# Kernel optimization log

Hardware: AMD Instinct MI355X
Metric: run time of the kernel (lower is better)

Reference implementation:

```python
import jax, jax.numpy as jnp
import numpy as np

EMB = 256
HEADS = 4
HD = EMB // HEADS
BS, SZ = 4, 64


def _layernorm(x, g, b, eps=1e-5):
    mu = jnp.mean(x, axis=-1, keepdims=True)
    var = jnp.mean((x - mu) ** 2, axis=-1, keepdims=True)
    return (x - mu) * jax.lax.rsqrt(var + eps) * g + b


def setup_inputs() -> dict:
    key = jax.random.key(0)
    ks = jax.random.split(key, 12)
    s = lambda k, shape, sc: jax.random.normal(k, shape, jnp.float32) * sc
    return {
        "x": s(ks[0], (BS, EMB, SZ, SZ), 1.0),
        "ln1_g": jnp.ones((EMB,), jnp.float32),
        "ln1_b": jnp.zeros((EMB,), jnp.float32),
        "wq": s(ks[1], (HD, HD), HD ** -0.5), "bq": jnp.zeros((HD,), jnp.float32),
        "wk": s(ks[2], (HD, HD), HD ** -0.5), "bk": jnp.zeros((HD,), jnp.float32),
        "wv": s(ks[3], (HD, HD), HD ** -0.5), "bv": jnp.zeros((HD,), jnp.float32),
        "wo": s(ks[4], (EMB, EMB), EMB ** -0.5), "bo": jnp.zeros((EMB,), jnp.float32),
        "ln2_g": jnp.ones((EMB,), jnp.float32),
        "ln2_b": jnp.zeros((EMB,), jnp.float32),
        "w1": s(ks[5], (EMB, EMB), EMB ** -0.5), "b1": jnp.zeros((EMB,), jnp.float32),
        "w2": s(ks[6], (EMB, EMB), EMB ** -0.5), "b2": jnp.zeros((EMB,), jnp.float32),
    }


def reference(x, ln1_g, ln1_b, wq, bq, wk, bk, wv, bv, wo, bo, ln2_g, ln2_b, w1, b1, w2, b2):
    bs, c, sz, _ = x.shape
    seq = sz * sz
    xt = x.reshape(bs, c, seq).swapaxes(1, 2)  # [b, s, c]
    xn = _layernorm(xt, ln1_g, ln1_b)
    # split heads: [b, h, s, d]
    h = xn.reshape(bs, seq, HEADS, HD).transpose(0, 2, 1, 3)
    q = h @ wq + bq
    k = h @ wk + bk
    v = h @ wv + bv
    scores = jnp.einsum("bhqd,bhkd->bhqk", q, k) / (HD ** 0.5)
    attn = jax.nn.softmax(scores, axis=-1)
    o = jnp.einsum("bhqk,bhkd->bhqd", attn, v)
    o = o.transpose(0, 2, 1, 3).reshape(bs, seq, c)
    o = o @ wo + bo
    av = o + xt  # residual 1
    ff = _layernorm(av, ln2_g, ln2_b) @ w1 + b1
    ff = jax.nn.gelu(ff, approximate=False) @ w2 + b2
    out = ff + av  # residual 2
    return out.swapaxes(1, 2).reshape(bs, c, sz, sz)
```

## Files before the change

kernel.cpp:

```cpp
#include <hip/hip_runtime.h>
#include <hip/hip_bf16.h>
#include <cstdint>

typedef __attribute__((ext_vector_type(8))) short short8;
typedef __attribute__((ext_vector_type(4))) short short4_;
typedef __attribute__((ext_vector_type(4))) float float4_;

#define MFMA16(a,b,c)  __builtin_amdgcn_mfma_f32_16x16x32_bf16(a,b,c,0,0,0)
#define MFMA16K16(a,b,c) __builtin_amdgcn_mfma_f32_16x16x16bf16_1k(a,b,c,0,0,0)
#define EXP2(x) __builtin_amdgcn_exp2f(x)

__device__ __forceinline__ short f2bs(float f) {
    union { float f; uint32_t u; } c;
    c.f = f;
    c.u += 0x7FFF + ((c.u >> 16) & 1);
    return (short)(c.u >> 16);
}
__device__ __forceinline__ float s2f(short s) {
    union { uint32_t u; float f; } c;
    c.u = ((uint32_t)(uint16_t)s) << 16;
    return c.f;
}

static const int EMB = 256;
static const int SEQ = 4096;
static const int TOK = 16384;

static const size_t SZO = 4194304;
static const size_t LSTRIDE = 65536;

#define QSCALE 0.18033688011112042f

__global__ __launch_bounds__(256) void repack_kernel(
    const float* wq, const float* wk, const float* wv,
    const float* wo, const float* w1, const float* w2,
    short* wqT, short* wkT, short* wvT, short* woT, short* w1T, short* w2T)
{
    int idx = blockIdx.x * 256 + threadIdx.x;
    if (idx < 3 * 4096) {
        int m = idx / 4096, r = idx % 4096;
        int n = r / 64, k = r % 64;
        const float* src = (m == 0) ? wq : (m == 1) ? wk : wv;
        short* dst = (m == 0) ? wqT : (m == 1) ? wkT : wvT;
        float v = src[k * 64 + n];
        if (m == 0) v *= QSCALE;
        dst[n * 64 + k] = f2bs(v);
    } else {
        int idx2 = idx - 3 * 4096;
        if (idx2 < 3 * 65536) {
            int m = idx2 / 65536, r = idx2 % 65536;
            int n = r / 256, k = r % 256;
            const float* src = (m == 0) ? wo : (m == 1) ? w1 : w2;
            short* dst = (m == 0) ? woT : (m == 1) ? w1T : w2T;
            dst[n * 256 + k] = f2bs(src[k * 256 + n]);
        }
    }
}

__global__ __launch_bounds__(256) void ln1_kernel(
    const float* x, const float* g, const float* bta,
    short* xn, short* xt)
{
    __shared__ float redS[4][32], redQ[4][32];
    int tid = threadIdx.x;
    int l = tid & 31;
    int p = tid >> 5;
    int t = blockIdx.x * 32 + l;
    int b = t >> 12, sp = t & 4095;
    const float* xb = x + (size_t)b * EMB * SEQ + (size_t)(p * 32) * SEQ + sp;

    float v[32];
    float sum = 0.f, ss = 0.f;
#pragma unroll
    for (int j = 0; j < 32; j++) {
        v[j] = xb[(size_t)j * SEQ];
        sum += v[j]; ss += v[j] * v[j];
    }
    sum += __shfl_xor(sum, 32);
    ss  += __shfl_xor(ss, 32);
    int w = tid >> 6;
    if ((tid & 32) == 0) { redS[w][l] = sum; redQ[w][l] = ss; }
    __syncthreads();
    float S = (redS[0][l] + redS[1][l]) + (redS[2][l] + redS[3][l]);
    float Q = (redQ[0][l] + redQ[1][l]) + (redQ[2][l] + redQ[3][l]);
    float mu = S * (1.f / 256.f);
    float var = Q * (1.f / 256.f) - mu * mu;
    float rs = rsqrtf(var + 1e-5f);

    short* xnr = xn + (size_t)t * 256 + p * 32;
    short* xtr = xt + (size_t)t * 256 + p * 32;
#pragma unroll
    for (int c = 0; c < 32; c += 8) {
        short8 ra, na;
#pragma unroll
        for (int j = 0; j < 8; j++) {
            float vv = v[c + j];
            ra[j] = f2bs(vv);
            na[j] = f2bs((vv - mu) * rs * g[p * 32 + c + j] + bta[p * 32 + c + j]);
        }
        *(short8*)(xtr + c) = ra;
        *(short8*)(xnr + c) = na;
    }
}

__global__ __launch_bounds__(256) void qkv_kernel(
    const short* xn, const short* wqT, const short* wkT, const short* wvT,
    const float* bq, const float* bk, const float* bv,
    short* qo, short* ko, short* vto)
{
    int tid = threadIdx.x;
    int w = tid >> 6, lane = tid & 63, quad = lane >> 4, l15 = lane & 15;
    int m0 = blockIdx.x * 64 + w * 16;
    int row = m0 + l15;
    int bb = row >> 12;
    int p = blockIdx.y;

    short8 a0[4], a1[4];
#pragma unroll
    for (int h = 0; h < 4; h++) {
        a0[h] = *(const short8*)(xn + (size_t)row * 256 + h * 64 + quad * 8);
        a1[h] = *(const short8*)(xn + (size_t)row * 256 + h * 64 + 32 + quad * 8);
    }

    const short* WT = (p == 0) ? wqT : (p == 1) ? wkT : wvT;
    const float* bias = (p == 0) ? bq : (p == 1) ? bk : bv;

    if (p < 2) {
        float bscale = (p == 0) ? QSCALE : 1.f;
        short* dst = (p == 0) ? qo : ko;
        int s0 = (m0 & 4095) + quad * 4;
#pragma unroll
        for (int nb = 0; nb < 4; nb++) {
            int col = nb * 16 + l15;
            short8 b0 = *(const short8*)(WT + col * 64 + quad * 8);
            short8 b1 = *(const short8*)(WT + col * 64 + 32 + quad * 8);
            float bvv = bias[col] * bscale;
#pragma unroll
            for (int h = 0; h < 4; h++) {
                float4_ acc = {bvv, bvv, bvv, bvv};
                acc = MFMA16(a0[h], b0, acc);
                acc = MFMA16(a1[h], b1, acc);
                size_t headbase = (size_t)(bb * 4 + h) * SEQ;
#pragma unroll
                for (int r = 0; r < 4; r++)
                    dst[(headbase + s0 + r) * 64 + col] = f2bs(acc[r]);
            }
        }
    } else {
        int sp0 = m0 & 4095;
#pragma unroll
        for (int nb = 0; nb < 4; nb++) {
            int colw = nb * 16 + l15;
            short8 b0 = *(const short8*)(WT + colw * 64 + quad * 8);
            short8 b1 = *(const short8*)(WT + colw * 64 + 32 + quad * 8);
            float4_ binit;
#pragma unroll
            for (int r = 0; r < 4; r++) binit[r] = bias[nb * 16 + quad * 4 + r];
#pragma unroll
            for (int h = 0; h < 4; h++) {
                float4_ acc = binit;
                acc = MFMA16(b0, a0[h], acc);
                acc = MFMA16(b1, a1[h], acc);
                size_t dbase = ((size_t)(bb * 4 + h) * 64 + nb * 16 + quad * 4) * SEQ;
#pragma unroll
                for (int r = 0; r < 4; r++)
                    vto[dbase + (size_t)r * SEQ + sp0 + l15] = f2bs(acc[r]);
            }
        }
    }
}

__global__ __attribute__((amdgpu_flat_work_group_size(256, 256),
                          amdgpu_waves_per_eu(4, 4)))
void flash_kernel(
    const short* q, const short* k, const short* vt,
    short* O0, short* Orest, float* lbase)
{
    __shared__ short K_lds[64 * 64];
    __shared__ short V_lds[64 * 64];

    int tid = threadIdx.x;
    int w = tid >> 6, lane = tid & 63, quad = lane >> 4, l15 = lane & 15;
    int qt = blockIdx.x, bh = blockIdx.y, grp = blockIdx.z;
    int span = 64 / gridDim.z;

    const short* qb = q + (size_t)bh * SEQ * 64;
    const short* kb = k + (size_t)bh * SEQ * 64 + (size_t)grp * span * 64 * 64;
    const short* vb = vt + (size_t)bh * 64 * SEQ + grp * span * 64;

    int qrow0 = qt * 128 + w * 32 + l15;
    int qrow1 = qrow0 + 16;
    short8 qA0 = *(const short8*)(qb + (size_t)qrow0 * 64 + quad * 8);
    short8 qA1 = *(const short8*)(qb + (size_t)qrow0 * 64 + 32 + quad * 8);
    short8 qB0 = *(const short8*)(qb + (size_t)qrow1 * 64 + quad * 8);
    short8 qB1 = *(const short8*)(qb + (size_t)qrow1 * 64 + 32 + quad * 8);

    float4_ oacc0[4], oacc1[4];
#pragma unroll
    for (int md = 0; md < 4; md++) {
        oacc0[md] = {0.f, 0.f, 0.f, 0.f};
        oacc1[md] = {0.f, 0.f, 0.f, 0.f};
    }
    float li0 = 0.f, li1 = 0.f;

    int srow = tid >> 2;
    int c0 = tid & 3;
    int sw = (srow & 7) ^ ((srow & 1) << 2);
    int rw = (l15 & 7) ^ ((l15 & 1) << 2);

    int dcA = (c0 ^ sw) << 3;
    int dcB = ((c0 + 4) ^ sw) << 3;

    short8 kr0 = *(const short8*)(kb + (size_t)srow * 64 + c0 * 8);
    short8 kr1 = *(const short8*)(kb + (size_t)srow * 64 + (c0 + 4) * 8);
    short8 vr0 = *(const short8*)(vb + (size_t)srow * SEQ + c0 * 8);
    short8 vr1 = *(const short8*)(vb + (size_t)srow * SEQ + (c0 + 4) * 8);

    for (int kt = 0; kt < span; kt++) {
        __syncthreads();
        *(short8*)&K_lds[srow * 64 + dcA] = kr0;
        *(short8*)&K_lds[srow * 64 + dcB] = kr1;
        *(short8*)&V_lds[srow * 64 + dcA] = vr0;
        *(short8*)&V_lds[srow * 64 + dcB] = vr1;
        if (kt + 1 < span) {
            kr0 = *(const short8*)(kb + (size_t)((kt + 1) * 64 + srow) * 64 + c0 * 8);
            kr1 = *(const short8*)(kb + (size_t)((kt + 1) * 64 + srow) * 64 + (c0 + 4) * 8);
            vr0 = *(const short8*)(vb + (size_t)srow * SEQ + (kt + 1) * 64 + c0 * 8);
            vr1 = *(const short8*)(vb + (size_t)srow * SEQ + (kt + 1) * 64 + (c0 + 4) * 8);
        }
        asm volatile("s_waitcnt lgkmcnt(0)" ::: "memory");
        __builtin_amdgcn_s_barrier();
        asm volatile("" ::: "memory");

        short4_ pf0[4], pf1[4];
#pragma unroll
        for (int nb = 0; nb < 4; nb++) {
            short8 k0 = *(const short8*)&K_lds[(nb * 16 + l15) * 64 + ((quad ^ rw) << 3)];
            short8 k1 = *(const short8*)&K_lds[(nb * 16 + l15) * 64 + (((quad + 4) ^ rw) << 3)];
            float4_ a = {0.f, 0.f, 0.f, 0.f};
            a = MFMA16(k0, qA0, a);
            a = MFMA16(k1, qA1, a);
            float4_ b = {0.f, 0.f, 0.f, 0.f};
            b = MFMA16(k0, qB0, b);
            b = MFMA16(k1, qB1, b);

            float p00 = EXP2(a[0]), p01 = EXP2(a[1]);
            float p02 = EXP2(a[2]), p03 = EXP2(a[3]);
            li0 += (p00 + p01) + (p02 + p03);
            float p10 = EXP2(b[0]), p11 = EXP2(b[1]);
            float p12 = EXP2(b[2]), p13 = EXP2(b[3]);
            li1 += (p10 + p11) + (p12 + p13);
            union { short4_ s; uint32_t u[2]; } pa, pb;
            asm("v_cvt_pk_bf16_f32 %0, %1, %2" : "=v"(pa.u[0]) : "v"(p00), "v"(p01));
            asm("v_cvt_pk_bf16_f32 %0, %1, %2" : "=v"(pa.u[1]) : "v"(p02), "v"(p03));
            asm("v_cvt_pk_bf16_f32 %0, %1, %2" : "=v"(pb.u[0]) : "v"(p10), "v"(p11));
            asm("v_cvt_pk_bf16_f32 %0, %1, %2" : "=v"(pb.u[1]) : "v"(p12), "v"(p13));
            pf0[nb] = pa.s;
            pf1[nb] = pb.s;
        }

        __builtin_amdgcn_s_setprio(1);
#pragma unroll
        for (int md = 0; md < 4; md++)
#pragma unroll
            for (int nb = 0; nb < 4; nb++) {
                int c = nb * 2 + (quad >> 1);
                short4_ vf = *(const short4_*)&V_lds[(md * 16 + l15) * 64 +
                                                     ((c ^ rw) << 3) + ((quad & 1) << 2)];
                oacc0[md] = MFMA16K16(vf, pf0[nb], oacc0[md]);
                oacc1[md] = MFMA16K16(vf, pf1[nb], oacc1[md]);
            }
        __builtin_amdgcn_s_setprio(0);
    }

    li0 += __shfl_xor(li0, 16);
    li0 += __shfl_xor(li0, 32);
    li1 += __shfl_xor(li1, 16);
    li1 += __shfl_xor(li1, 32);

    short* Op = grp ? (Orest + (size_t)(grp - 1) * SZO) : O0;
    float* lp = lbase + (size_t)grp * LSTRIDE;
    if (quad == 0) {
        lp[bh * 4096 + qrow0] = li0;
        lp[bh * 4096 + qrow1] = li1;
    }

    size_t ob0 = ((size_t)bh * 4096 + qrow0) * 64;
    size_t ob1 = ((size_t)bh * 4096 + qrow1) * 64;
#pragma unroll
    for (int md = 0; md < 4; md++) {
        short4_ pk0, pk1;
#pragma unroll
        for (int r = 0; r < 4; r++) {
            pk0[r] = f2bs(oacc0[md][r]);
            pk1[r] = f2bs(oacc1[md][r]);
        }
        *(short4_*)(Op + ob0 + md * 16 + quad * 4) = pk0;
        *(short4_*)(Op + ob1 + md * 16 + quad * 4) = pk1;
    }
}

__global__ __launch_bounds__(256) void combine_kernel(
    const short* O0, const short* Orest, const float* lb,
    short* Oout, int np)
{
    int g = blockIdx.x * 256 + threadIdx.x;
    int qi = g >> 4;
    short4_ a = *(const short4_*)(O0 + (size_t)g * 4);
    float l = lb[qi];
    float4_ acc = {s2f(a[0]), s2f(a[1]), s2f(a[2]), s2f(a[3])};
    for (int j = 1; j < np; j++) {
        short4_ b = *(const short4_*)(Orest + (size_t)(j - 1) * SZO + (size_t)g * 4);
        l += lb[(size_t)j * LSTRIDE + qi];
#pragma unroll
        for (int jj = 0; jj < 4; jj++) acc[jj] += s2f(b[jj]);
    }
    float inv = 1.f / l;
    short4_ pk;
#pragma unroll
    for (int j = 0; j < 4; j++) pk[j] = f2bs(acc[j] * inv);
    *(short4_*)(Oout + (size_t)g * 4) = pk;
}

__global__ __launch_bounds__(256) void mlp_kernel(
    const short* O0, const short* Orest, const float* lb, int np,
    const short* woT, const short* w1T, const short* w2T,
    const float* bo, const float* b1, const float* b2,
    const float* g2, const float* be2,
    const short* xt, float* outf)
{
    __shared__ __align__(16) char smem[3 * 8448 + 128];
    short* av = (short*)smem;
    short* x2 = (short*)(smem + 8448);
    short* ff = (short*)(smem + 16896);
    float* stats = (float*)(smem + 25344);
    float* T = (float*)smem;

    int tid = threadIdx.x;
    int w = tid >> 6, lane = tid & 63, quad = lane >> 4, l15 = lane & 15;
    int m0 = blockIdx.x * 16;
    int n0 = w * 64;
    int arow = m0 + l15;
    int bbA = arow >> 12, spA = arow & 4095;

    float invh[4];
    if (np) {
#pragma unroll
        for (int h = 0; h < 4; h++) {
            size_t li = (size_t)(bbA * 4 + h) * 4096 + spA;
            float s = lb[li];
            for (int j = 1; j < np; j++) s += lb[(size_t)j * LSTRIDE + li];
            invh[h] = 1.f / s;
        }
    }

    float4_ acc[4];
#pragma unroll
    for (int nb = 0; nb < 4; nb++) {
        float bvv = bo[n0 + nb * 16 + l15];
        acc[nb] = {bvv, bvv, bvv, bvv};
    }
    for (int kc = 0; kc < 8; kc++) {
        int h = kc >> 1;
        int off = (kc & 1) * 32 + quad * 8;
        size_t obase = ((size_t)(bbA * 4 + h) * 4096 + spA) * 64 + off;
        short8 a;
        if (np) {
            short8 a0v = *(const short8*)(O0 + obase);
            float f[8];
#pragma unroll
            for (int jj = 0; jj < 8; jj++) f[jj] = s2f(a0v[jj]);
            for (int j = 1; j < np; j++) {
                short8 apv = *(const short8*)(Orest + (size_t)(j - 1) * SZO + obase);
#pragma unroll
                for (int jj = 0; jj < 8; jj++) f[jj] += s2f(apv[jj]);
            }
            float iv = invh[h];
            union { short8 s; uint32_t u[4]; } pa;
#pragma unroll
            for (int jj = 0; jj < 4; jj++) {
                float f0 = f[2 * jj] * iv;
                float f1 = f[2 * jj + 1] * iv;
                asm("v_cvt_pk_bf16_f32 %0, %1, %2" : "=v"(pa.u[jj]) : "v"(f0), "v"(f1));
            }
            a = pa.s;
        } else {
            a = *(const short8*)(O0 + obase);
        }
#pragma unroll
        for (int nb = 0; nb < 4; nb++) {
            short8 b = *(const short8*)(woT + (size_t)(n0 + nb * 16 + l15) * 256 + kc * 32 + quad * 8);
            acc[nb] = MFMA16(a, b, acc[nb]);
        }
    }
#pragma unroll
    for (int nb = 0; nb < 4; nb++) {
        int col = n0 + nb * 16 + l15;
#pragma unroll
        for (int r = 0; r < 4; r++) {
            size_t t = (size_t)m0 + quad * 4 + r;
            av[(quad * 4 + r) * 264 + col] = f2bs(acc[nb][r] + s2f(xt[t * 256 + col]));
        }
    }
    __syncthreads();

    {
        int row = tid >> 4, sub = tid & 15;
        float sum = 0.f, ss = 0.f;
        short8 v0 = *(const short8*)&av[row * 264 + sub * 16];
        short8 v1 = *(const short8*)&av[row * 264 + sub * 16 + 8];
#pragma unroll
        for (int j = 0; j < 8; j++) {
            float a = s2f(v0[j]), b = s2f(v1[j]);
            sum += a + b; ss += a * a + b * b;
        }
#pragma unroll
        for (int off = 1; off < 16; off <<= 1) {
            sum += __shfl_xor(sum, off);
            ss += __shfl_xor(ss, off);
        }
        if (sub == 0) {
            float mu = sum * (1.f / 256.f);
            float var = ss * (1.f / 256.f) - mu * mu;
            stats[row] = mu;
            stats[16 + row] = rsqrtf(var + 1e-5f);
        }
    }
    __syncthreads();

    {
        int row = tid >> 4, sub = tid & 15;
        float mu = stats[row], rs = stats[16 + row];
#pragma unroll
        for (int j = 0; j < 16; j += 4) {
            int c = sub * 16 + j;
            short4_ rv = *(const short4_*)&av[row * 264 + c];
            short4_ pk;
#pragma unroll
            for (int i = 0; i < 4; i++)
                pk[i] = f2bs((s2f(rv[i]) - mu) * rs * g2[c + i] + be2[c + i]);
            *(short4_*)&x2[row * 264 + c] = pk;
        }
    }
    __syncthreads();

#pragma unroll
    for (int nb = 0; nb < 4; nb++) {
        float bvv = b1[n0 + nb * 16 + l15];
        acc[nb] = {bvv, bvv, bvv, bvv};
    }
    for (int kc = 0; kc < 8; kc++) {
        short8 a = *(const short8*)&x2[l15 * 264 + kc * 32 + quad * 8];
#pragma unroll
        for (int nb = 0; nb < 4; nb++) {
            short8 b = *(const short8*)(w1T + (size_t)(n0 + nb * 16 + l15) * 256 + kc * 32 + quad * 8);
            acc[nb] = MFMA16(a, b, acc[nb]);
        }
    }
#pragma unroll
    for (int nb = 0; nb < 4; nb++) {
        int col = n0 + nb * 16 + l15;
#pragma unroll
        for (int r = 0; r < 4; r++) {
            float v = acc[nb][r];
            v = 0.5f * v * (1.f + erff(v * 0.70710678118f));
            ff[(quad * 4 + r) * 264 + col] = f2bs(v);
        }
    }
    __syncthreads();

#pragma unroll
    for (int nb = 0; nb < 4; nb++) {
        float bvv = b2[n0 + nb * 16 + l15];
        acc[nb] = {bvv, bvv, bvv, bvv};
    }
    for (int kc = 0; kc < 8; kc++) {
        short8 a = *(const short8*)&ff[l15 * 264 + kc * 32 + quad * 8];
#pragma unroll
        for (int nb = 0; nb < 4; nb++) {
            short8 b = *(const short8*)(w2T + (size_t)(n0 + nb * 16 + l15) * 256 + kc * 32 + quad * 8);
            acc[nb] = MFMA16(a, b, acc[nb]);
        }
    }
    float vout[4][4];
#pragma unroll
    for (int nb = 0; nb < 4; nb++) {
        int col = n0 + nb * 16 + l15;
#pragma unroll
        for (int r = 0; r < 4; r++)
            vout[nb][r] = acc[nb][r] + s2f(av[(quad * 4 + r) * 264 + col]);
    }
    __syncthreads();

    float* tw = T + w * 1040;
#pragma unroll
    for (int nb = 0; nb < 4; nb++)
#pragma unroll
        for (int r = 0; r < 4; r++)
            tw[(quad * 4 + r) * 65 + nb * 16 + l15] = vout[nb][r];

    int bb = m0 >> 12;
    int spb = m0 & 4095;
    float* dst = outf + ((size_t)bb * 256 + n0 + lane) * SEQ + spb;
#pragma unroll
    for (int j = 0; j < 16; j += 4) {
        float4_ pk = {tw[(j + 0) * 65 + lane], tw[(j + 1) * 65 + lane],
                      tw[(j + 2) * 65 + lane], tw[(j + 3) * 65 + lane]};
        *(float4_*)(dst + j) = pk;
    }
}

extern "C" void kernel_launch(void* const* d_in, const int* in_sizes, int n_in,
                              void* d_out, int out_size, void* d_ws, size_t ws_size,
                              hipStream_t stream)
{
    const float* x     = (const float*)d_in[0];
    const float* ln1_g = (const float*)d_in[1];
    const float* ln1_b = (const float*)d_in[2];
    const float* wq    = (const float*)d_in[3];
    const float* bq    = (const float*)d_in[4];
    const float* wk    = (const float*)d_in[5];
    const float* bk    = (const float*)d_in[6];
    const float* wv    = (const float*)d_in[7];
    const float* bv    = (const float*)d_in[8];
    const float* wo    = (const float*)d_in[9];
    const float* bo    = (const float*)d_in[10];
    const float* ln2_g = (const float*)d_in[11];
    const float* ln2_b = (const float*)d_in[12];
    const float* w1    = (const float*)d_in[13];
    const float* b1    = (const float*)d_in[14];
    const float* w2    = (const float*)d_in[15];
    const float* b2    = (const float*)d_in[16];

    char* ws = (char*)d_ws;
    const size_t SZ_BF = (size_t)TOK * 256 * 2;

    short* wqT = (short*)(ws + 0);
    short* wkT = (short*)(ws + 8192);
    short* wvT = (short*)(ws + 16384);
    short* woT = (short*)(ws + 24576);
    short* w1T = (short*)(ws + 155648);
    short* w2T = (short*)(ws + 286720);
    char* base = ws + 524288;

    short* xt  = (short*)(base);
    short* kbuf= (short*)(base + SZ_BF);
    short* vtb = (short*)(base + 2 * SZ_BF);

    const size_t need2_fb = 524288 + 3 * SZ_BF + 524288 + SZ_BF;
    const size_t need2_fu = need2_fb + SZ_BF;
    const size_t need4_fb = 524288 + 3 * SZ_BF + 1048576 + 3 * SZ_BF;
    const size_t need4_fu = need4_fb + SZ_BF;

    int nz, fuse;
    if (ws_size >= need4_fb)      { nz = 4; fuse = (ws_size >= need4_fu); }
    else if (ws_size >= need2_fb) { nz = 2; fuse = (ws_size >= need2_fu); }
    else                          { nz = 1; fuse = 0; }

    float* lbase;
    short* Orest;
    short* O0w;
    if (nz == 4) {
        lbase = (float*)(base + 3 * SZ_BF);
        Orest = (short*)(base + 3 * SZ_BF + 1048576);
        O0w   = Orest + 3 * SZO;
    } else {
        lbase = (float*)(base + 3 * SZ_BF);
        Orest = (short*)(base + 3 * SZ_BF + 524288);
        O0w   = Orest + SZO;
    }

    short* qb  = (short*)d_out;
    short* xn  = (short*)((char*)d_out + SZ_BF);
    short* O0  = fuse ? O0w : xn;
    short* Onrm= vtb;

    repack_kernel<<<816, 256, 0, stream>>>(wq, wk, wv, wo, w1, w2,
                                           wqT, wkT, wvT, woT, w1T, w2T);
    ln1_kernel<<<TOK / 32, 256, 0, stream>>>(x, ln1_g, ln1_b, xn, xt);
    qkv_kernel<<<dim3(TOK / 64, 3), 256, 0, stream>>>(xn, wqT, wkT, wvT, bq, bk, bv,
                                                      qb, kbuf, vtb);
    flash_kernel<<<dim3(32, 16, nz), 256, 0, stream>>>(qb, kbuf, vtb, O0, Orest, lbase);
    if (fuse) {
        mlp_kernel<<<TOK / 16, 256, 0, stream>>>(O0, Orest, lbase, nz,
                                                 woT, w1T, w2T, bo, b1, b2,
                                                 ln2_g, ln2_b, xt, (float*)d_out);
    } else {
        combine_kernel<<<4096, 256, 0, stream>>>(O0, Orest, lbase, Onrm, nz);
        mlp_kernel<<<TOK / 16, 256, 0, stream>>>(Onrm, Orest, lbase, 0,
                                                 woT, w1T, w2T, bo, b1, b2,
                                                 ln2_g, ln2_b, xt, (float*)d_out);
    }
}
```

Before: 267.3 us.

## Fuse LayerNorm1 with QKV projection, staging normalized rows in LDS

Merges the ln1 and qkv kernels into one. Each block normalizes 64 tokens, writes the bf16 normalized rows to padded shared memory instead of global memory, then computes Q, K and V from LDS in one launch rather than three grid slices. This removes a global write and re-read of xn plus one launch. In exchange each thread now holds 64 floats in registers and the Q/K/V work is serialized per block, which may lower occupancy and parallelism.

Result: no change. 263.3 us (-1.5%).

```diff
diff --git a/kernel.cpp b/kernel.cpp
--- a/kernel.cpp
+++ b/kernel.cpp
@@ -57,29 +57,32 @@
     }
 }
 
-__global__ __launch_bounds__(256) void ln1_kernel(
+__global__ __attribute__((amdgpu_flat_work_group_size(256, 256),
+                          amdgpu_waves_per_eu(1, 4)))
+void ln1qkv_kernel(
     const float* x, const float* g, const float* bta,
-    short* xn, short* xt)
+    const short* wqT, const short* wkT, const short* wvT,
+    const float* bq, const float* bk, const float* bv,
+    short* xt, short* qo, short* ko, short* vto)
 {
-    __shared__ float redS[4][32], redQ[4][32];
+    __shared__ short xn_lds[64 * 264];
+    __shared__ float redS[4][64], redQ[4][64];
+
     int tid = threadIdx.x;
-    int l = tid & 31;
-    int p = tid >> 5;
-    int t = blockIdx.x * 32 + l;
+    int l = tid & 63;
+    int cp = tid >> 6;
+    int t = blockIdx.x * 64 + l;
     int b = t >> 12, sp = t & 4095;
-    const float* xb = x + (size_t)b * EMB * SEQ + (size_t)(p * 32) * SEQ + sp;
-
-    float v[32];
+    const float* xb = x + (size_t)b * EMB * SEQ + (size_t)(cp * 64) * SEQ + sp;
+
+    float v[64];
+#pragma unroll
+    for (int j = 0; j < 64; j++) v[j] = xb[(size_t)j * SEQ];
     float sum = 0.f, ss = 0.f;
 #pragma unroll
-    for (int j = 0; j < 32; j++) {
-        v[j] = xb[(size_t)j * SEQ];
-        sum += v[j]; ss += v[j] * v[j];
-    }
-    sum += __shfl_xor(sum, 32);
-    ss  += __shfl_xor(ss, 32);
-    int w = tid >> 6;
-    if ((tid & 32) == 0) { redS[w][l] = sum; redQ[w][l] = ss; }
+    for (int j = 0; j < 64; j++) { sum += v[j]; ss += v[j] * v[j]; }
+    redS[cp][l] = sum;
+    redQ[cp][l] = ss;
     __syncthreads();
     float S = (redS[0][l] + redS[1][l]) + (redS[2][l] + redS[3][l]);
     float Q = (redQ[0][l] + redQ[1][l]) + (redQ[2][l] + redQ[3][l]);
@@ -87,84 +90,81 @@
     float var = Q * (1.f / 256.f) - mu * mu;
     float rs = rsqrtf(var + 1e-5f);
 
-    short* xnr = xn + (size_t)t * 256 + p * 32;
-    short* xtr = xt + (size_t)t * 256 + p * 32;
-#pragma unroll
-    for (int c = 0; c < 32; c += 8) {
+    short* xtr = xt + (size_t)t * 256 + cp * 64;
+    short* xnr = xn_lds + l * 264 + cp * 64;
+#pragma unroll
+    for (int c = 0; c < 64; c += 8) {
         short8 ra, na;
 #pragma unroll
         for (int j = 0; j < 8; j++) {
             float vv = v[c + j];
             ra[j] = f2bs(vv);
-            na[j] = f2bs((vv - mu) * rs * g[p * 32 + c + j] + bta[p * 32 + c + j]);
+            na[j] = f2bs((vv - mu) * rs * g[cp * 64 + c + j] + bta[cp * 64 + c + j]);
         }
         *(short8*)(xtr + c) = ra;
         *(short8*)(xnr + c) = na;
     }
-}
-
-__global__ __launch_bounds__(256) void qkv_kernel(
-    const short* xn, const short* wqT, const short* wkT, const short* wvT,
-    const float* bq, const float* bk, const float* bv,
-    short* qo, short* ko, short* vto)
-{
-    int tid = threadIdx.x;
+    __syncthreads();
+
     int w = tid >> 6, lane = tid & 63, quad = lane >> 4, l15 = lane & 15;
     int m0 = blockIdx.x * 64 + w * 16;
     int row = m0 + l15;
     int bb = row >> 12;
-    int p = blockIdx.y;
-
+
+    const short* arow = xn_lds + (w * 16 + l15) * 264;
     short8 a0[4], a1[4];
 #pragma unroll
     for (int h = 0; h < 4; h++) {
-        a0[h] = *(const short8*)(xn + (size_t)row * 256 + h * 64 + quad * 8);
-        a1[h] = *(const short8*)(xn + (size_t)row * 256 + h * 64 + 32 + quad * 8);
-    }
-
-    const short* WT = (p == 0) ? wqT : (p == 1) ? wkT : wvT;
-    const float* bias = (p == 0) ? bq : (p == 1) ? bk : bv;
-
-    if (p < 2) {
-        float bscale = (p == 0) ? QSCALE : 1.f;
-        short* dst = (p == 0) ? qo : ko;
-        int s0 = (m0 & 4095) + quad * 4;
-#pragma unroll
-        for (int nb = 0; nb < 4; nb++) {
-            int col = nb * 16 + l15;
-            short8 b0 = *(const short8*)(WT + col * 64 + quad * 8);
-            short8 b1 = *(const short8*)(WT + col * 64 + 32 + quad * 8);
-            float bvv = bias[col] * bscale;
-#pragma unroll
-            for (int h = 0; h < 4; h++) {
-                float4_ acc = {bvv, bvv, bvv, bvv};
-                acc = MFMA16(a0[h], b0, acc);
-                acc = MFMA16(a1[h], b1, acc);
-                size_t headbase = (size_t)(bb * 4 + h) * SEQ;
-#pragma unroll
-                for (int r = 0; r < 4; r++)
-                    dst[(headbase + s0 + r) * 64 + col] = f2bs(acc[r]);
+        a0[h] = *(const short8*)(arow + h * 64 + quad * 8);
+        a1[h] = *(const short8*)(arow + h * 64 + 32 + quad * 8);
+    }
+
+#pragma unroll
+    for (int p = 0; p < 3; p++) {
+        const short* WT = (p == 0) ? wqT : (p == 1) ? wkT : wvT;
+        const float* bias = (p == 0) ? bq : (p == 1) ? bk : bv;
+
+        if (p < 2) {
+            float bscale = (p == 0) ? QSCALE : 1.f;
+            short* dst = (p == 0) ? qo : ko;
+            int s0 = (m0 & 4095) + quad * 4;
+#pragma unroll
+            for (int nb = 0; nb < 4; nb++) {
+                int col = nb * 16 + l15;
+                short8 b0 = *(const short8*)(WT + col * 64 + quad * 8);
+                short8 b1 = *(const short8*)(WT + col * 64 + 32 + quad * 8);
+                float bvv = bias[col] * bscale;
+#pragma unroll
+                for (int h = 0; h < 4; h++) {
+                    float4_ acc = {bvv, bvv, bvv, bvv};
+                    acc = MFMA16(a0[h], b0, acc);
+                    acc = MFMA16(a1[h], b1, acc);
+                    size_t headbase = (size_t)(bb * 4 + h) * SEQ;
+#pragma unroll
+                    for (int r = 0; r < 4; r++)
+                        dst[(headbase + s0 + r) * 64 + col] = f2bs(acc[r]);
+                }
             }
-        }
-    } else {
-        int sp0 = m0 & 4095;
-#pragma unroll
-        for (int nb = 0; nb < 4; nb++) {
-            int colw = nb * 16 + l15;
-            short8 b0 = *(const short8*)(WT + colw * 64 + quad * 8);
-            short8 b1 = *(const short8*)(WT + colw * 64 + 32 + quad * 8);
-            float4_ binit;
-#pragma unroll
-            for (int r = 0; r < 4; r++) binit[r] = bias[nb * 16 + quad * 4 + r];
-#pragma unroll
-            for (int h = 0; h < 4; h++) {
-                float4_ acc = binit;
-                acc = MFMA16(b0, a0[h], acc);
-                acc = MFMA16(b1, a1[h], acc);
-                size_t dbase = ((size_t)(bb * 4 + h) * 64 + nb * 16 + quad * 4) * SEQ;
-#pragma unroll
-                for (int r = 0; r < 4; r++)
-                    vto[dbase + (size_t)r * SEQ + sp0 + l15] = f2bs(acc[r]);
+        } else {
+            int sp0 = m0 & 4095;
+#pragma unroll
+            for (int nb = 0; nb < 4; nb++) {
+                int colw = nb * 16 + l15;
+                short8 b0 = *(const short8*)(WT + colw * 64 + quad * 8);
+                short8 b1 = *(const short8*)(WT + colw * 64 + 32 + quad * 8);
+                float4_ binit;
+#pragma unroll
+                for (int r = 0; r < 4; r++) binit[r] = bias[nb * 16 + quad * 4 + r];
+#pragma unroll
+                for (int h = 0; h < 4; h++) {
+                    float4_ acc = binit;
+                    acc = MFMA16(b0, a0[h], acc);
+                    acc = MFMA16(b1, a1[h], acc);
+                    size_t dbase = ((size_t)(bb * 4 + h) * 64 + nb * 16 + quad * 4) * SEQ;
+#pragma unroll
+                    for (int r = 0; r < 4; r++)
+                        vto[dbase + (size_t)r * SEQ + sp0 + l15] = f2bs(acc[r]);
+                }
             }
         }
     }
@@ -571,15 +571,15 @@
     }
 
     short* qb  = (short*)d_out;
-    short* xn  = (short*)((char*)d_out + SZ_BF);
-    short* O0  = fuse ? O0w : xn;
+    short* upper = (short*)((char*)d_out + SZ_BF);
+    short* O0  = fuse ? O0w : upper;
     short* Onrm= vtb;
 
     repack_kernel<<<816, 256, 0, stream>>>(wq, wk, wv, wo, w1, w2,
                                            wqT, wkT, wvT, woT, w1T, w2T);
-    ln1_kernel<<<TOK / 32, 256, 0, stream>>>(x, ln1_g, ln1_b, xn, xt);
-    qkv_kernel<<<dim3(TOK / 64, 3), 256, 0, stream>>>(xn, wqT, wkT, wvT, bq, bk, bv,
-                                                      qb, kbuf, vtb);
+    ln1qkv_kernel<<<TOK / 64, 256, 0, stream>>>(x, ln1_g, ln1_b,
+                                                wqT, wkT, wvT, bq, bk, bv,
+                                                xt, qb, kbuf, vtb);
     flash_kernel<<<dim3(32, 16, nz), 256, 0, stream>>>(qb, kbuf, vtb, O0, Orest, lbase);
     if (fuse) {
         mlp_kernel<<<TOK / 16, 256, 0, stream>>>(O0, Orest, lbase, nz,
```
